# Optimization experiments

Measured on AMD Instinct MI355X. Metric: run time of the kernel, lower is better.

Reference implementation:

```python
import jax, jax.numpy as jnp
import numpy as np
from jax import lax

B, C, H, W = 8, 36, 256, 256
E, K, TD = 6, 2, 32
HID = C * 2  # ffn_expansion_factor = 2
EPS = 1e-10


def _conv3x3(x, w):
    # x: [B, Cin, H, W], w: [Cout, Cin, 3, 3], stride 1, pad 1, no bias
    return lax.conv_general_dilated(
        x, w, window_strides=(1, 1), padding=[(1, 1), (1, 1)],
        dimension_numbers=("NCHW", "OIHW", "NCHW"))


def _cv_squared(v):
    # torch .var() is unbiased (ddof=1)
    return jnp.var(v, ddof=1) / (jnp.mean(v) ** 2 + EPS)


def setup_inputs() -> dict:
    key = jax.random.key(0)
    ks = jax.random.split(key, 10)
    s = 0.05
    return {
        "x": jax.random.normal(ks[0], (B, C, H, W), dtype=jnp.float32),
        "time": jax.random.normal(ks[1], (B, TD), dtype=jnp.float32),
        # FeatureWiseAffine: Linear(time_dim -> expert_dim*2)
        "time_w": jax.random.normal(ks[2], (TD, HID), dtype=jnp.float32) * s,
        "time_b": jnp.zeros((HID,), dtype=jnp.float32),
        # gate: Linear(72,72) -> LeakyReLU -> Linear(72,6)
        "gate_w1": jax.random.normal(ks[3], (HID, HID), dtype=jnp.float32) * s,
        "gate_b1": jnp.zeros((HID,), dtype=jnp.float32),
        "gate_w2": jax.random.normal(ks[4], (HID, E), dtype=jnp.float32) * s,
        "gate_b2": jnp.zeros((E,), dtype=jnp.float32),
        # per-expert conv weights, stacked over experts
        "conv1_w": jax.random.normal(ks[5], (E, HID, C, 3, 3), dtype=jnp.float32) * s,
        "conv2_w": jax.random.normal(ks[6], (E, C, HID, 3, 3), dtype=jnp.float32) * s,
    }


def reference(x, time, time_w, time_b, gate_w1, gate_b1, gate_w2, gate_b2,
              conv1_w, conv2_w):
    # ---- gating (eval mode: no noise) ----
    # NOTE: source names are swapped: self.maxpool = AdaptiveAvgPool2d(1),
    # self.meanpool = AdaptiveMaxPool2d(1). Order preserved: [avg, max].
    avg_vec = jnp.mean(x, axis=(2, 3))              # [B, C]
    max_vec = jnp.max(x, axis=(2, 3))               # [B, C]
    v = jnp.concatenate([avg_vec, max_vec], axis=1)  # [B, 2C]
    v = v + time @ time_w + time_b                   # FeatureWiseAffine (additive)
    h = v @ gate_w1 + gate_b1
    h = jnp.where(h > 0, h, 0.01 * h)                # LeakyReLU(0.01)
    clean_logits = h @ gate_w2 + gate_b2             # [B, E]

    top_vals, top_idx = lax.top_k(clean_logits, min(K + 1, E))
    topk_gates = jax.nn.softmax(top_vals[:, :K], axis=1)     # [B, K]
    rows = jnp.arange(B)[:, None]
    gates = jnp.zeros_like(clean_logits).at[rows, top_idx[:, :K]].set(topk_gates)

    importance = gates.sum(axis=0)                           # [E]
    load = (gates > 0).sum(axis=0).astype(jnp.float32)       # [E] (eval path)
    loss = (_cv_squared(importance) + _cv_squared(load)) * 0.01

    # ---- dense equivalent of sparse dispatch / expert / gate-weighted combine ----
    # y[b] = sum_e gates[b,e] * expert_e(x[b]); zero gates contribute nothing,
    # identical to SparseDispatcher's gather -> conv -> scatter-add combine.
    y = jnp.zeros_like(x)
    for e in range(E):
        t = _conv3x3(x, conv1_w[e])
        t = jax.nn.gelu(t, approximate=False)   # F.gelu default = exact erf
        t = _conv3x3(t, conv2_w[e])
        y = y + gates[:, e].reshape(B, 1, 1, 1) * t
    return y, loss
```

## Files before the change

kernel.cpp:

```cpp
#include <hip/hip_runtime.h>
#include <hip/hip_bf16.h>
#include <math.h>

#define BB 8
#define CCH 36
#define HH 256
#define WW 256
#define EE 6
#define TDIM 32
#define HID 72
#define WS_GATES (BB*CCH*2)
#define WT1_OFF 4096
#define WT2_OFF (4096 + 368640)

#define TW 16
#define TH 8
#define XR 12
#define XC 20
#define TR 10
#define TC 18

typedef __attribute__((ext_vector_type(8))) short bf16x8;
typedef __attribute__((ext_vector_type(4))) float f32x4;

static __device__ __forceinline__ unsigned short f2bf(float f) {
  __hip_bfloat16 h = __float2bfloat16(f);
  return *(unsigned short*)&h;
}
static __device__ __forceinline__ float gelu_fast(float x) {
  float n2u = x * (-1.5957691216f - 0.0713548162f * x * x);
  float r = __builtin_amdgcn_rcpf(1.f + __expf(n2u));
  return x * r;
}

__global__ __launch_bounds__(256) void poolwx_kernel(const float* __restrict__ x,
                                                     const float* __restrict__ w1,
                                                     const float* __restrict__ w2,
                                                     float* __restrict__ ws,
                                                     unsigned short* __restrict__ wt1,
                                                     unsigned short* __restrict__ wt2) {
  if (blockIdx.x < 288) {
    const int bc = blockIdx.x;
    const float* p = x + (size_t)bc * (HH * WW);
    float s = 0.f, m = -INFINITY;
    for (int i = threadIdx.x; i < (HH * WW) / 4; i += 256) {
      float4 v = ((const float4*)p)[i];
      s += v.x + v.y + v.z + v.w;
      m = fmaxf(m, fmaxf(fmaxf(v.x, v.y), fmaxf(v.z, v.w)));
    }
    for (int off = 32; off; off >>= 1) {
      s += __shfl_down(s, off);
      m = fmaxf(m, __shfl_down(m, off));
    }
    __shared__ float ss[4], sm[4];
    int wid = threadIdx.x >> 6, lane = threadIdx.x & 63;
    if (lane == 0) { ss[wid] = s; sm[wid] = m; }
    __syncthreads();
    if (threadIdx.x == 0) {
      float S = ss[0] + ss[1] + ss[2] + ss[3];
      float M = fmaxf(fmaxf(sm[0], sm[1]), fmaxf(sm[2], sm[3]));
      ws[bc] = S * (1.f / (HH * WW));
      ws[BB * CCH + bc] = M;
    }
    return;
  }
  int i = (blockIdx.x - 288) * 256 + threadIdx.x;
  const int n1 = 360 * 512;
  if (i < n1) {
    int j = i & 7;
    int lane = (i >> 3) & 63;
    int f = i >> 9;
    int mt = f % 5;  f /= 5;
    int kc = f % 4;  f /= 4;
    int dx = f % 3;  int e = f / 3;
    int co = mt * 16 + (lane & 15);
    int k = kc * 32 + (lane >> 4) * 8 + j;
    int dy = k / 40, ci = k % 40;
    float v = 0.f;
    if (co < HID && k < 120 && ci < CCH)
      v = w1[(((size_t)(e * HID + co) * CCH + ci) * 3 + dy) * 3 + dx];
    wt1[i] = f2bf(v);
  }
  const int n2 = 378 * 512;
  if (i < n2) {
    int j = i & 7;
    int lane = (i >> 3) & 63;
    int f = i >> 9;
    int mt = f % 3;  f /= 3;
    int kc = f % 7;  f /= 7;
    int dx = f % 3;  int e = f / 3;
    int co = mt * 16 + (lane & 15);
    int k = kc * 32 + (lane >> 4) * 8 + j;
    int dy = k / 72, ci = k % 72;
    float v = 0.f;
    if (co < CCH && k < 216)
      v = w2[(((size_t)(e * CCH + co) * HID + ci) * 3 + dy) * 3 + dx];
    wt2[i] = f2bf(v);
  }
}

__global__ void gate_kernel(const float* __restrict__ time,
                            const float* __restrict__ time_w,
                            const float* __restrict__ time_b,
                            const float* __restrict__ w1, const float* __restrict__ b1,
                            const float* __restrict__ w2, const float* __restrict__ b2,
                            float* __restrict__ ws, float* __restrict__ loss_out) {
  __shared__ float v[BB * HID];
  __shared__ float h[BB * HID];
  __shared__ float logits[BB * EE];
  const int t = threadIdx.x;
  const float* avg = ws;
  const float* mx = ws + BB * CCH;
  for (int i = t; i < BB * HID; i += blockDim.x) {
    int b = i / HID, c = i % HID;
    float base = (c < CCH) ? avg[b * CCH + c] : mx[b * CCH + (c - CCH)];
    float acc = time_b[c];
    for (int k = 0; k < TDIM; k++) acc += time[b * TDIM + k] * time_w[k * HID + c];
    v[i] = base + acc;
  }
  __syncthreads();
  for (int i = t; i < BB * HID; i += blockDim.x) {
    int b = i / HID, c = i % HID;
    float acc = b1[c];
    for (int k = 0; k < HID; k++) acc += v[b * HID + k] * w1[k * HID + c];
    h[i] = acc > 0.f ? acc : 0.01f * acc;
  }
  __syncthreads();
  for (int i = t; i < BB * EE; i += blockDim.x) {
    int b = i / EE, e = i % EE;
    float acc = b2[e];
    for (int k = 0; k < HID; k++) acc += h[b * HID + k] * w2[k * EE + e];
    logits[i] = acc;
  }
  __syncthreads();
  if (t == 0) {
    float imp[EE], ld[EE];
    for (int e = 0; e < EE; e++) { imp[e] = 0.f; ld[e] = 0.f; }
    for (int b = 0; b < BB; b++) {
      int i1 = -1, i2 = -1;
      float v1 = -1e30f, v2 = -1e30f;
      for (int e = 0; e < EE; e++) {
        float lv = logits[b * EE + e];
        if (lv > v1) { v2 = v1; i2 = i1; v1 = lv; i1 = e; }
        else if (lv > v2) { v2 = lv; i2 = e; }
      }
      float e2 = expf(v2 - v1);
      float g1 = 1.f / (1.f + e2), g2 = e2 / (1.f + e2);
      for (int e = 0; e < EE; e++) ws[WS_GATES + b * EE + e] = 0.f;
      ws[WS_GATES + b * EE + i1] = g1;
      ws[WS_GATES + b * EE + i2] = g2;
      imp[i1] += g1; imp[i2] += g2;
      ld[i1] += 1.f; ld[i2] += 1.f;
    }
    float loss = 0.f;
    {
      float m = 0.f; for (int e = 0; e < EE; e++) m += imp[e]; m /= EE;
      float var = 0.f; for (int e = 0; e < EE; e++) { float d = imp[e] - m; var += d * d; }
      var /= (EE - 1);
      loss += var / (m * m + 1e-10f);
      m = 0.f; for (int e = 0; e < EE; e++) m += ld[e]; m /= EE;
      var = 0.f; for (int e = 0; e < EE; e++) { float d = ld[e] - m; var += d * d; }
      var /= (EE - 1);
      loss += var / (m * m + 1e-10f);
    }
    loss_out[0] = 0.01f * loss;
  }
}

__global__ __launch_bounds__(256, 3) void conv_kernel(
    const float* __restrict__ x,
    const unsigned short* __restrict__ wt1,
    const unsigned short* __restrict__ wt2,
    const float* __restrict__ wsg,
    float* __restrict__ y) {
  __shared__ __align__(16) char lds[48000];
  char* xsB = lds;
  char* tsB = lds + 19200;

  const int tid = threadIdx.x;
  const int w = tid >> 6;
  const int lane = tid & 63;
  const int l15 = lane & 15;
  const int kl = lane >> 4;
  const int b = blockIdx.y;
  const int tileId = (blockIdx.x & 7) * 64 + (blockIdx.x >> 3);
  const int tx0 = (tileId & 15) * TW;
  const int ty0 = (tileId >> 4) * TH;
  const size_t xbase = (size_t)b * (CCH * HH * WW);

  int eids[2] = {0, 0};
  float gvals[2] = {0.f, 0.f};
  int ne = 0;
  for (int e = 0; e < EE; e++) {
    float g = wsg[b * EE + e];
    if (g != 0.f && ne < 2) { eids[ne] = e; gvals[ne] = g; ne++; }
  }
  ne = __builtin_amdgcn_readfirstlane(ne);
  const int e0 = __builtin_amdgcn_readfirstlane(eids[0]);
  const int e1 = __builtin_amdgcn_readfirstlane(eids[1]);
  const float g0 = __int_as_float(__builtin_amdgcn_readfirstlane(__float_as_int(gvals[0])));
  const float g1 = __int_as_float(__builtin_amdgcn_readfirstlane(__float_as_int(gvals[1])));

  if (tid < XR * XC) {
    const int xr = tid / XC, xc = tid - (tid / XC) * XC;
    const int gy = ty0 - 2 + xr, gx = tx0 - 2 + xc;
    const bool valid = ((unsigned)gy < (unsigned)HH) && ((unsigned)gx < (unsigned)WW);
    const float* xp = x + xbase + (size_t)(gy * WW + gx);
    char* dstb = xsB + (xr * XC + xc) * 16;
#pragma unroll
    for (int c8 = 0; c8 < 5; c8++) {
      unsigned int pk[4];
#pragma unroll
      for (int q = 0; q < 4; q++) {
        int ci0 = c8 * 8 + q * 2, ci1 = ci0 + 1;
        float v0 = (ci0 < CCH && valid) ? xp[(size_t)ci0 << 16] : 0.f;
        float v1 = (ci1 < CCH && valid) ? xp[(size_t)ci1 << 16] : 0.f;
        pk[q] = (unsigned)f2bf(v0) | ((unsigned)f2bf(v1) << 16);
      }
      *(uint4*)(dstb + c8 * 3840) = make_uint4(pk[0], pk[1], pk[2], pk[3]);
    }
  }

  int vimg[3], pst[3], tsoff[3], pb1[3];
#pragma unroll
  for (int i = 0; i < 3; i++) {
    int p = (w + 4 * i) * 16 + l15;
    int tr = p / TC, tc = p - tr * TC;
    pst[i] = (p < TR * TC) ? 1 : 0;
    int trc = tr < (TR - 1) ? tr : (TR - 1);
    pb1[i] = trc * 320 + tc * 16;
    tsoff[i] = trc * 288 + tc * 16;
    int gy = ty0 - 1 + tr, gx = tx0 - 1 + tc;
    vimg[i] = (pst[i] && (unsigned)gy < (unsigned)HH && (unsigned)gx < (unsigned)WW) ? 1 : 0;
  }
  int b1a[4][3];
#pragma unroll
  for (int kc = 0; kc < 4; kc++) {
    int k0 = kc * 32 + kl * 8;
    int d = (k0 >= 80) ? 2 : (k0 >= 40 ? 1 : 0);
    int xkc = (k0 < 120) ? (((k0 - 40 * d) >> 3) * 3840 + d * 320) : 0;
#pragma unroll
    for (int i = 0; i < 3; i++) b1a[kc][i] = pb1[i] + xkc;
  }
  int tsStore[3];
#pragma unroll
  for (int i = 0; i < 3; i++) tsStore[i] = tsoff[i] + (kl >> 1) * 2880 + (kl & 1) * 8;

  int b2a[7][2];
#pragma unroll
  for (int kc = 0; kc < 7; kc++) {
    int k0 = kc * 32 + kl * 8;
    int d = (k0 >= 144) ? 2 : (k0 >= 72 ? 1 : 0);
    int tkc = (k0 < 216) ? (((k0 - 72 * d) >> 3) * 2880 + d * 288) : 0;
#pragma unroll
    for (int i = 0; i < 2; i++) b2a[kc][i] = (w + 4 * i) * 288 + l15 * 16 + tkc;
  }

  const int lob = lane * 8;

  f32x4 yacc[2][3];
#pragma unroll
  for (int i = 0; i < 2; i++)
#pragma unroll
    for (int mt = 0; mt < 3; mt++) yacc[i][mt] = (f32x4){0.f, 0.f, 0.f, 0.f};

  __syncthreads();

#pragma unroll
  for (int ei = 0; ei < 2; ei++) {
    if (ei >= ne) break;
    const float gv = ei ? g1 : g0;
    const unsigned short* w1p = wt1 + (ei ? e1 : e0) * 30720;
    const unsigned short* w2p = wt2 + (ei ? e1 : e0) * 32256;

    f32x4 acc[3][5];
#pragma unroll
    for (int i = 0; i < 3; i++)
#pragma unroll
      for (int mt = 0; mt < 5; mt++) acc[i][mt] = (f32x4){0.f, 0.f, 0.f, 0.f};

    bf16x8 aA[5], aB[5];
#pragma unroll
    for (int mt = 0; mt < 5; mt++) aA[mt] = *(const bf16x8*)(w1p + mt * 512 + lob);

#pragma unroll
    for (int jj = 0; jj < 12; jj++) {
      if (jj < 11) {
#pragma unroll
        for (int mt = 0; mt < 5; mt++)
          ((jj & 1) ? aA : aB)[mt] = *(const bf16x8*)(w1p + ((jj + 1) * 5 + mt) * 512 + lob);
      }
      const int kc = jj & 3;
      const int dxo = (jj >> 2) * 16;
      bf16x8 bv[3];
#pragma unroll
      for (int i = 0; i < 3; i++)
        bv[i] = *(const bf16x8*)(xsB + b1a[kc][i] + dxo);
      __builtin_amdgcn_s_setprio(1);
#pragma unroll
      for (int mt = 0; mt < 5; mt++) {
        bf16x8 av = ((jj & 1) ? aB : aA)[mt];
#pragma unroll
        for (int i = 0; i < 3; i++)
          acc[i][mt] = __builtin_amdgcn_mfma_f32_16x16x32_bf16(av, bv[i], acc[i][mt], 0, 0, 0);
      }
      __builtin_amdgcn_s_setprio(0);
    }

    bf16x8 c0[3], c1[3], c2[3];
#pragma unroll
    for (int mt = 0; mt < 3; mt++) {
      c0[mt] = *(const bf16x8*)(w2p + mt * 512 + lob);
      c1[mt] = *(const bf16x8*)(w2p + (3 + mt) * 512 + lob);
    }

#pragma unroll
    for (int i = 0; i < 3; i++) {
      if (pst[i]) {
#pragma unroll
        for (int mt = 0; mt < 5; mt++) {
          float v0 = vimg[i] ? gv * gelu_fast(acc[i][mt].x) : 0.f;
          float v1 = vimg[i] ? gv * gelu_fast(acc[i][mt].y) : 0.f;
          float v2 = vimg[i] ? gv * gelu_fast(acc[i][mt].z) : 0.f;
          float v3 = vimg[i] ? gv * gelu_fast(acc[i][mt].w) : 0.f;
          unsigned int lo = (unsigned)f2bf(v0) | ((unsigned)f2bf(v1) << 16);
          unsigned int hi = (unsigned)f2bf(v2) | ((unsigned)f2bf(v3) << 16);
          *(uint2*)(tsB + tsStore[i] + mt * 5760) = make_uint2(lo, hi);
        }
      }
    }
    __syncthreads();

#pragma unroll
    for (int jj = 0; jj < 21; jj++) {
      if (jj < 19) {
#pragma unroll
        for (int mt = 0; mt < 3; mt++) {
          bf16x8 v = *(const bf16x8*)(w2p + ((jj + 2) * 3 + mt) * 512 + lob);
          if ((jj % 3) == 0) c2[mt] = v;
          else if ((jj % 3) == 1) c0[mt] = v;
          else c1[mt] = v;
        }
      }
      const int kc = jj % 7;
      const int dxo = (jj / 7) * 16;
      bf16x8 bv[2];
#pragma unroll
      for (int i = 0; i < 2; i++)
        bv[i] = *(const bf16x8*)(tsB + b2a[kc][i] + dxo);
      __builtin_amdgcn_s_setprio(1);
#pragma unroll
      for (int mt = 0; mt < 3; mt++) {
        bf16x8 av = ((jj % 3) == 0) ? c0[mt] : ((jj % 3) == 1) ? c1[mt] : c2[mt];
#pragma unroll
        for (int i = 0; i < 2; i++)
          yacc[i][mt] = __builtin_amdgcn_mfma_f32_16x16x32_bf16(av, bv[i], yacc[i][mt], 0, 0, 0);
      }
      __builtin_amdgcn_s_setprio(0);
    }
    __syncthreads();
  }

#pragma unroll
  for (int i = 0; i < 2; i++) {
    int row = w + 4 * i;
#pragma unroll
    for (int mt = 0; mt < 3; mt++) {
#pragma unroll
      for (int r = 0; r < 4; r++) {
        int co = mt * 16 + kl * 4 + r;
        if (co < CCH) {
          float v = (r == 0) ? yacc[i][mt].x : (r == 1) ? yacc[i][mt].y
                  : (r == 2) ? yacc[i][mt].z : yacc[i][mt].w;
          y[xbase + ((size_t)co << 16) + (size_t)((ty0 + row) * WW + tx0 + l15)] = v;
        }
      }
    }
  }
}

extern "C" void kernel_launch(void* const* d_in, const int* in_sizes, int n_in,
                              void* d_out, int out_size, void* d_ws, size_t ws_size,
                              hipStream_t stream) {
  const float* x      = (const float*)d_in[0];
  const float* time   = (const float*)d_in[1];
  const float* time_w = (const float*)d_in[2];
  const float* time_b = (const float*)d_in[3];
  const float* gw1    = (const float*)d_in[4];
  const float* gb1    = (const float*)d_in[5];
  const float* gw2    = (const float*)d_in[6];
  const float* gb2    = (const float*)d_in[7];
  const float* w1     = (const float*)d_in[8];
  const float* w2     = (const float*)d_in[9];
  float* out = (float*)d_out;
  float* ws  = (float*)d_ws;
  unsigned short* wt1 = (unsigned short*)((char*)d_ws + WT1_OFF);
  unsigned short* wt2 = (unsigned short*)((char*)d_ws + WT2_OFF);

  hipLaunchKernelGGL(poolwx_kernel, dim3(288 + 756), dim3(256), 0, stream,
                     x, w1, w2, ws, wt1, wt2);
  hipLaunchKernelGGL(gate_kernel, dim3(1), dim3(128), 0, stream,
                     time, time_w, time_b, gw1, gb1, gw2, gb2,
                     ws, out + (size_t)(out_size - 1));
  hipLaunchKernelGGL(conv_kernel, dim3(512, BB), dim3(256), 0, stream,
                     x, wt1, wt2, ws + WS_GATES, out);
}
```

Baseline: 236.8 us.

## Stage expert conv weights in LDS via global_load_lds and alias x/t buffers

Weights for both convolutions are no longer read from global memory into registers by every wave. They are now staged in phases into a shared LDS weight buffer with direct global-to-LDS loads, and the MFMA loops read their A fragments from LDS. The x tile and the GELU intermediate tile now share one LDS region, so x is reloaded from global memory for each selected expert. This removes redundant per-wave global weight traffic and register double-buffering, at the cost of many extra __syncthreads between phases, loss of load/compute overlap, and a second global read of the x tile.

```diff
diff --git a/kernel.cpp b/kernel.cpp
--- a/kernel.cpp
+++ b/kernel.cpp
@@ -173,9 +173,10 @@
     const unsigned short* __restrict__ wt2,
     const float* __restrict__ wsg,
     float* __restrict__ y) {
-  __shared__ __align__(16) char lds[48000];
+  __shared__ __align__(16) char lds[49280];
   char* xsB = lds;
-  char* tsB = lds + 19200;
+  char* tsB = lds;
+  char* wB  = lds + 28800;
 
   const int tid = threadIdx.x;
   const int w = tid >> 6;
@@ -201,26 +202,6 @@
   const float g0 = __int_as_float(__builtin_amdgcn_readfirstlane(__float_as_int(gvals[0])));
   const float g1 = __int_as_float(__builtin_amdgcn_readfirstlane(__float_as_int(gvals[1])));
 
-  if (tid < XR * XC) {
-    const int xr = tid / XC, xc = tid - (tid / XC) * XC;
-    const int gy = ty0 - 2 + xr, gx = tx0 - 2 + xc;
-    const bool valid = ((unsigned)gy < (unsigned)HH) && ((unsigned)gx < (unsigned)WW);
-    const float* xp = x + xbase + (size_t)(gy * WW + gx);
-    char* dstb = xsB + (xr * XC + xc) * 16;
-#pragma unroll
-    for (int c8 = 0; c8 < 5; c8++) {
-      unsigned int pk[4];
-#pragma unroll
-      for (int q = 0; q < 4; q++) {
-        int ci0 = c8 * 8 + q * 2, ci1 = ci0 + 1;
-        float v0 = (ci0 < CCH && valid) ? xp[(size_t)ci0 << 16] : 0.f;
-        float v1 = (ci1 < CCH && valid) ? xp[(size_t)ci1 << 16] : 0.f;
-        pk[q] = (unsigned)f2bf(v0) | ((unsigned)f2bf(v1) << 16);
-      }
-      *(uint4*)(dstb + c8 * 3840) = make_uint4(pk[0], pk[1], pk[2], pk[3]);
-    }
-  }
-
   int vimg[3], pst[3], tsoff[3], pb1[3];
 #pragma unroll
   for (int i = 0; i < 3; i++) {
@@ -256,7 +237,7 @@
     for (int i = 0; i < 2; i++) b2a[kc][i] = (w + 4 * i) * 288 + l15 * 16 + tkc;
   }
 
-  const int lob = lane * 8;
+  const int lob = lane * 16;
 
   f32x4 yacc[2][3];
 #pragma unroll
@@ -264,14 +245,42 @@
 #pragma unroll
     for (int mt = 0; mt < 3; mt++) yacc[i][mt] = (f32x4){0.f, 0.f, 0.f, 0.f};
 
-  __syncthreads();
-
-#pragma unroll
   for (int ei = 0; ei < 2; ei++) {
     if (ei >= ne) break;
     const float gv = ei ? g1 : g0;
-    const unsigned short* w1p = wt1 + (ei ? e1 : e0) * 30720;
-    const unsigned short* w2p = wt2 + (ei ? e1 : e0) * 32256;
+    const char* w1p = (const char*)(wt1 + (ei ? e1 : e0) * 30720);
+    const char* w2p = (const char*)(wt2 + (ei ? e1 : e0) * 32256);
+
+    __syncthreads();
+
+#pragma unroll
+    for (int j = 0; j < 5; j++) {
+      int c = w + 4 * j;
+      __builtin_amdgcn_global_load_lds(
+          (const __attribute__((address_space(1))) void*)(w1p + c * 1024 + lob),
+          (__attribute__((address_space(3))) void*)(wB + c * 1024), 16, 0, 0);
+    }
+
+    if (tid < XR * XC) {
+      const int xr = tid / XC, xc = tid - (tid / XC) * XC;
+      const int gy = ty0 - 2 + xr, gx = tx0 - 2 + xc;
+      const bool valid = ((unsigned)gy < (unsigned)HH) && ((unsigned)gx < (unsigned)WW);
+      const float* xp = x + xbase + (size_t)(gy * WW + gx);
+      char* dstb = xsB + (xr * XC + xc) * 16;
+#pragma unroll
+      for (int c8 = 0; c8 < 5; c8++) {
+        unsigned int pk[4];
+#pragma unroll
+        for (int q = 0; q < 4; q++) {
+          int ci0 = c8 * 8 + q * 2, ci1 = ci0 + 1;
+          float v0 = (ci0 < CCH && valid) ? xp[(size_t)ci0 << 16] : 0.f;
+          float v1 = (ci1 < CCH && valid) ? xp[(size_t)ci1 << 16] : 0.f;
+          pk[q] = (unsigned)f2bf(v0) | ((unsigned)f2bf(v1) << 16);
+        }
+        *(uint4*)(dstb + c8 * 3840) = make_uint4(pk[0], pk[1], pk[2], pk[3]);
+      }
+    }
+    __syncthreads();
 
     f32x4 acc[3][5];
 #pragma unroll
@@ -279,39 +288,50 @@
 #pragma unroll
       for (int mt = 0; mt < 5; mt++) acc[i][mt] = (f32x4){0.f, 0.f, 0.f, 0.f};
 
-    bf16x8 aA[5], aB[5];
-#pragma unroll
-    for (int mt = 0; mt < 5; mt++) aA[mt] = *(const bf16x8*)(w1p + mt * 512 + lob);
-
-#pragma unroll
-    for (int jj = 0; jj < 12; jj++) {
-      if (jj < 11) {
+#pragma unroll
+    for (int ph = 0; ph < 3; ph++) {
+      if (ph > 0) {
+        __syncthreads();
+#pragma unroll
+        for (int j = 0; j < 5; j++) {
+          int c = w + 4 * j;
+          __builtin_amdgcn_global_load_lds(
+              (const __attribute__((address_space(1))) void*)(w1p + ph * 20480 + c * 1024 + lob),
+              (__attribute__((address_space(3))) void*)(wB + c * 1024), 16, 0, 0);
+        }
+        __syncthreads();
+      }
+#pragma unroll
+      for (int q = 0; q < 4; q++) {
+        const int jj = ph * 4 + q;
+        const int kc = jj & 3;
+        const int dxo = (jj >> 2) * 16;
+        bf16x8 bv[3];
+#pragma unroll
+        for (int i = 0; i < 3; i++)
+          bv[i] = *(const bf16x8*)(xsB + b1a[kc][i] + dxo);
+        bf16x8 av[5];
 #pragma unroll
         for (int mt = 0; mt < 5; mt++)
-          ((jj & 1) ? aA : aB)[mt] = *(const bf16x8*)(w1p + ((jj + 1) * 5 + mt) * 512 + lob);
-      }
-      const int kc = jj & 3;
-      const int dxo = (jj >> 2) * 16;
-      bf16x8 bv[3];
-#pragma unroll
-      for (int i = 0; i < 3; i++)
-        bv[i] = *(const bf16x8*)(xsB + b1a[kc][i] + dxo);
-      __builtin_amdgcn_s_setprio(1);
-#pragma unroll
-      for (int mt = 0; mt < 5; mt++) {
-        bf16x8 av = ((jj & 1) ? aB : aA)[mt];
-#pragma unroll
-        for (int i = 0; i < 3; i++)
-          acc[i][mt] = __builtin_amdgcn_mfma_f32_16x16x32_bf16(av, bv[i], acc[i][mt], 0, 0, 0);
-      }
-      __builtin_amdgcn_s_setprio(0);
-    }
-
-    bf16x8 c0[3], c1[3], c2[3];
-#pragma unroll
-    for (int mt = 0; mt < 3; mt++) {
-      c0[mt] = *(const bf16x8*)(w2p + mt * 512 + lob);
-      c1[mt] = *(const bf16x8*)(w2p + (3 + mt) * 512 + lob);
+          av[mt] = *(const bf16x8*)(wB + (q * 5 + mt) * 1024 + lob);
+        __builtin_amdgcn_s_setprio(1);
+#pragma unroll
+        for (int mt = 0; mt < 5; mt++)
+#pragma unroll
+          for (int i = 0; i < 3; i++)
+            acc[i][mt] = __builtin_amdgcn_mfma_f32_16x16x32_bf16(av[mt], bv[i], acc[i][mt], 0, 0, 0);
+        __builtin_amdgcn_s_setprio(0);
+      }
+    }
+
+    __syncthreads();
+#pragma unroll
+    for (int j = 0; j < 5; j++) {
+      int c = w + 4 * j;
+      if (c < 18)
+        __builtin_amdgcn_global_load_lds(
+            (const __attribute__((address_space(1))) void*)(w2p + c * 1024 + lob),
+            (__attribute__((address_space(3))) void*)(wB + c * 1024), 16, 0, 0);
     }
 
 #pragma unroll
@@ -332,33 +352,44 @@
     __syncthreads();
 
 #pragma unroll
-    for (int jj = 0; jj < 21; jj++) {
-      if (jj < 19) {
-#pragma unroll
-        for (int mt = 0; mt < 3; mt++) {
-          bf16x8 v = *(const bf16x8*)(w2p + ((jj + 2) * 3 + mt) * 512 + lob);
-          if ((jj % 3) == 0) c2[mt] = v;
-          else if ((jj % 3) == 1) c0[mt] = v;
-          else c1[mt] = v;
+    for (int ph = 0; ph < 4; ph++) {
+      if (ph > 0) {
+        __syncthreads();
+        const int cnt = (ph == 3) ? 9 : 18;
+#pragma unroll
+        for (int j = 0; j < 5; j++) {
+          int c = w + 4 * j;
+          if (c < cnt)
+            __builtin_amdgcn_global_load_lds(
+                (const __attribute__((address_space(1))) void*)(w2p + (ph * 18 + c) * 1024 + lob),
+                (__attribute__((address_space(3))) void*)(wB + c * 1024), 16, 0, 0);
         }
-      }
-      const int kc = jj % 7;
-      const int dxo = (jj / 7) * 16;
-      bf16x8 bv[2];
-#pragma unroll
-      for (int i = 0; i < 2; i++)
-        bv[i] = *(const bf16x8*)(tsB + b2a[kc][i] + dxo);
-      __builtin_amdgcn_s_setprio(1);
-#pragma unroll
-      for (int mt = 0; mt < 3; mt++) {
-        bf16x8 av = ((jj % 3) == 0) ? c0[mt] : ((jj % 3) == 1) ? c1[mt] : c2[mt];
+        __syncthreads();
+      }
+      const int nq = (ph == 3) ? 3 : 6;
+#pragma unroll
+      for (int q = 0; q < 6; q++) {
+        if (q >= nq) break;
+        const int jj = ph * 6 + q;
+        const int kc = jj % 7;
+        const int dxo = (jj / 7) * 16;
+        bf16x8 bv[2];
 #pragma unroll
         for (int i = 0; i < 2; i++)
-          yacc[i][mt] = __builtin_amdgcn_mfma_f32_16x16x32_bf16(av, bv[i], yacc[i][mt], 0, 0, 0);
-      }
-      __builtin_amdgcn_s_setprio(0);
-    }
-    __syncthreads();
+          bv[i] = *(const bf16x8*)(tsB + b2a[kc][i] + dxo);
+        bf16x8 av[3];
+#pragma unroll
+        for (int mt = 0; mt < 3; mt++)
+          av[mt] = *(const bf16x8*)(wB + (q * 3 + mt) * 1024 + lob);
+        __builtin_amdgcn_s_setprio(1);
+#pragma unroll
+        for (int mt = 0; mt < 3; mt++)
+#pragma unroll
+          for (int i = 0; i < 2; i++)
+            yacc[i][mt] = __builtin_amdgcn_mfma_f32_16x16x32_bf16(av[mt], bv[i], yacc[i][mt], 0, 0, 0);
+        __builtin_amdgcn_s_setprio(0);
+      }
+    }
   }
 
 #pragma unroll
```

Result: slower. 531.0 us (+124.2%).

## Stage expert weight fragments through double-buffered LDS shared by all waves

Applied to the files above, without the earlier changes.

Weight fragments used to be loaded per wave straight from global memory into registers. They are now loaded cooperatively by the four waves into a double-buffered LDS region and read back from LDS by every wave. The x tile and the GELU intermediate now share one LDS buffer, so the x tile is reloaded for each active expert. The aim is to cut redundant global and L2 weight traffic across waves. The cost is extra LDS reads, a __syncthreads in every pipeline stage, and a second x-tile load per block.

```diff
diff --git a/kernel.cpp b/kernel.cpp
--- a/kernel.cpp
+++ b/kernel.cpp
@@ -173,9 +173,10 @@
     const unsigned short* __restrict__ wt2,
     const float* __restrict__ wsg,
     float* __restrict__ y) {
-  __shared__ __align__(16) char lds[48000];
+  __shared__ __align__(16) char lds[49280];
   char* xsB = lds;
-  char* tsB = lds + 19200;
+  char* tsB = lds;
+  char* wB  = lds + 28800;
 
   const int tid = threadIdx.x;
   const int w = tid >> 6;
@@ -201,26 +202,6 @@
   const float g0 = __int_as_float(__builtin_amdgcn_readfirstlane(__float_as_int(gvals[0])));
   const float g1 = __int_as_float(__builtin_amdgcn_readfirstlane(__float_as_int(gvals[1])));
 
-  if (tid < XR * XC) {
-    const int xr = tid / XC, xc = tid - (tid / XC) * XC;
-    const int gy = ty0 - 2 + xr, gx = tx0 - 2 + xc;
-    const bool valid = ((unsigned)gy < (unsigned)HH) && ((unsigned)gx < (unsigned)WW);
-    const float* xp = x + xbase + (size_t)(gy * WW + gx);
-    char* dstb = xsB + (xr * XC + xc) * 16;
-#pragma unroll
-    for (int c8 = 0; c8 < 5; c8++) {
-      unsigned int pk[4];
-#pragma unroll
-      for (int q = 0; q < 4; q++) {
-        int ci0 = c8 * 8 + q * 2, ci1 = ci0 + 1;
-        float v0 = (ci0 < CCH && valid) ? xp[(size_t)ci0 << 16] : 0.f;
-        float v1 = (ci1 < CCH && valid) ? xp[(size_t)ci1 << 16] : 0.f;
-        pk[q] = (unsigned)f2bf(v0) | ((unsigned)f2bf(v1) << 16);
-      }
-      *(uint4*)(dstb + c8 * 3840) = make_uint4(pk[0], pk[1], pk[2], pk[3]);
-    }
-  }
-
   int vimg[3], pst[3], tsoff[3], pb1[3];
 #pragma unroll
   for (int i = 0; i < 3; i++) {
@@ -256,7 +237,7 @@
     for (int i = 0; i < 2; i++) b2a[kc][i] = (w + 4 * i) * 288 + l15 * 16 + tkc;
   }
 
-  const int lob = lane * 8;
+  const int lob16 = lane * 16;
 
   f32x4 yacc[2][3];
 #pragma unroll
@@ -264,14 +245,46 @@
 #pragma unroll
     for (int mt = 0; mt < 3; mt++) yacc[i][mt] = (f32x4){0.f, 0.f, 0.f, 0.f};
 
-  __syncthreads();
-
-#pragma unroll
+  bf16x8 r0, r1, r2;
+
   for (int ei = 0; ei < 2; ei++) {
     if (ei >= ne) break;
     const float gv = ei ? g1 : g0;
-    const unsigned short* w1p = wt1 + (ei ? e1 : e0) * 30720;
-    const unsigned short* w2p = wt2 + (ei ? e1 : e0) * 32256;
+    const char* w1p = (const char*)(wt1 + (ei ? e1 : e0) * 30720);
+    const char* w2p = (const char*)(wt2 + (ei ? e1 : e0) * 32256);
+
+    if (tid < XR * XC) {
+      const int xr = tid / XC, xc = tid - (tid / XC) * XC;
+      const int gy = ty0 - 2 + xr, gx = tx0 - 2 + xc;
+      const bool valid = ((unsigned)gy < (unsigned)HH) && ((unsigned)gx < (unsigned)WW);
+      const float* xp = x + xbase + (size_t)(gy * WW + gx);
+      char* dstb = xsB + (xr * XC + xc) * 16;
+#pragma unroll
+      for (int c8 = 0; c8 < 5; c8++) {
+        unsigned int pk[4];
+#pragma unroll
+        for (int q = 0; q < 4; q++) {
+          int ci0 = c8 * 8 + q * 2, ci1 = ci0 + 1;
+          float v0 = (ci0 < CCH && valid) ? xp[(size_t)ci0 << 16] : 0.f;
+          float v1 = (ci1 < CCH && valid) ? xp[(size_t)ci1 << 16] : 0.f;
+          pk[q] = (unsigned)f2bf(v0) | ((unsigned)f2bf(v1) << 16);
+        }
+        *(uint4*)(dstb + c8 * 3840) = make_uint4(pk[0], pk[1], pk[2], pk[3]);
+      }
+    }
+    {
+      int c0 = w, c1 = w + 4, c2 = w + 8;
+      r0 = *(const bf16x8*)(w1p + c0 * 1024 + lob16);
+      r1 = *(const bf16x8*)(w1p + c1 * 1024 + lob16);
+      if (c2 < 10) r2 = *(const bf16x8*)(w1p + c2 * 1024 + lob16);
+      *(bf16x8*)(wB + c0 * 1024 + lob16) = r0;
+      *(bf16x8*)(wB + c1 * 1024 + lob16) = r1;
+      if (c2 < 10) *(bf16x8*)(wB + c2 * 1024 + lob16) = r2;
+      r0 = *(const bf16x8*)(w1p + (10 + c0) * 1024 + lob16);
+      r1 = *(const bf16x8*)(w1p + (10 + c1) * 1024 + lob16);
+      if (c2 < 10) r2 = *(const bf16x8*)(w1p + (10 + c2) * 1024 + lob16);
+    }
+    __syncthreads();
 
     f32x4 acc[3][5];
 #pragma unroll
@@ -279,41 +292,62 @@
 #pragma unroll
       for (int mt = 0; mt < 5; mt++) acc[i][mt] = (f32x4){0.f, 0.f, 0.f, 0.f};
 
-    bf16x8 aA[5], aB[5];
-#pragma unroll
-    for (int mt = 0; mt < 5; mt++) aA[mt] = *(const bf16x8*)(w1p + mt * 512 + lob);
-
-#pragma unroll
-    for (int jj = 0; jj < 12; jj++) {
-      if (jj < 11) {
+#pragma unroll
+    for (int p = 0; p < 6; p++) {
+      {
+        char* dst = wB + ((p + 1) & 1) * 10240;
+        const int nfr = (p < 5) ? 10 : 9;
+        int c0 = w, c1 = w + 4, c2 = w + 8;
+        *(bf16x8*)(dst + c0 * 1024 + lob16) = r0;
+        *(bf16x8*)(dst + c1 * 1024 + lob16) = r1;
+        if (c2 < nfr) *(bf16x8*)(dst + c2 * 1024 + lob16) = r2;
+      }
+      {
+        int c0 = w, c1 = w + 4, c2 = w + 8;
+        if (p < 4) {
+          r0 = *(const bf16x8*)(w1p + ((p + 2) * 10 + c0) * 1024 + lob16);
+          r1 = *(const bf16x8*)(w1p + ((p + 2) * 10 + c1) * 1024 + lob16);
+          if (c2 < 10) r2 = *(const bf16x8*)(w1p + ((p + 2) * 10 + c2) * 1024 + lob16);
+        } else {
+          r0 = *(const bf16x8*)(w2p + ((p - 4) * 9 + c0) * 1024 + lob16);
+          r1 = *(const bf16x8*)(w2p + ((p - 4) * 9 + c1) * 1024 + lob16);
+          if (c2 < 9) r2 = *(const bf16x8*)(w2p + ((p - 4) * 9 + c2) * 1024 + lob16);
+        }
+      }
+      const char* wb = wB + (p & 1) * 10240;
+#pragma unroll
+      for (int s = 0; s < 2; s++) {
+        const int jj = 2 * p + s;
+        const int kc = jj & 3;
+        const int dxo = (jj >> 2) * 16;
+        bf16x8 bv[3];
+#pragma unroll
+        for (int i = 0; i < 3; i++)
+          bv[i] = *(const bf16x8*)(xsB + b1a[kc][i] + dxo);
+        bf16x8 av[5];
 #pragma unroll
         for (int mt = 0; mt < 5; mt++)
-          ((jj & 1) ? aA : aB)[mt] = *(const bf16x8*)(w1p + ((jj + 1) * 5 + mt) * 512 + lob);
-      }
-      const int kc = jj & 3;
-      const int dxo = (jj >> 2) * 16;
-      bf16x8 bv[3];
-#pragma unroll
-      for (int i = 0; i < 3; i++)
-        bv[i] = *(const bf16x8*)(xsB + b1a[kc][i] + dxo);
-      __builtin_amdgcn_s_setprio(1);
-#pragma unroll
-      for (int mt = 0; mt < 5; mt++) {
-        bf16x8 av = ((jj & 1) ? aB : aA)[mt];
-#pragma unroll
-        for (int i = 0; i < 3; i++)
-          acc[i][mt] = __builtin_amdgcn_mfma_f32_16x16x32_bf16(av, bv[i], acc[i][mt], 0, 0, 0);
-      }
-      __builtin_amdgcn_s_setprio(0);
-    }
-
-    bf16x8 c0[3], c1[3], c2[3];
-#pragma unroll
-    for (int mt = 0; mt < 3; mt++) {
-      c0[mt] = *(const bf16x8*)(w2p + mt * 512 + lob);
-      c1[mt] = *(const bf16x8*)(w2p + (3 + mt) * 512 + lob);
-    }
-
+          av[mt] = *(const bf16x8*)(wb + (s * 5 + mt) * 1024 + lob16);
+        __builtin_amdgcn_s_setprio(1);
+#pragma unroll
+        for (int mt = 0; mt < 5; mt++)
+#pragma unroll
+          for (int i = 0; i < 3; i++)
+            acc[i][mt] = __builtin_amdgcn_mfma_f32_16x16x32_bf16(av[mt], bv[i], acc[i][mt], 0, 0, 0);
+        __builtin_amdgcn_s_setprio(0);
+      }
+      __syncthreads();
+    }
+
+    {
+      int c0 = w, c1 = w + 4, c2 = w + 8;
+      *(bf16x8*)(wB + 10240 + c0 * 1024 + lob16) = r0;
+      *(bf16x8*)(wB + 10240 + c1 * 1024 + lob16) = r1;
+      if (c2 < 9) *(bf16x8*)(wB + 10240 + c2 * 1024 + lob16) = r2;
+      r0 = *(const bf16x8*)(w2p + (18 + c0) * 1024 + lob16);
+      r1 = *(const bf16x8*)(w2p + (18 + c1) * 1024 + lob16);
+      if (c2 < 9) r2 = *(const bf16x8*)(w2p + (18 + c2) * 1024 + lob16);
+    }
 #pragma unroll
     for (int i = 0; i < 3; i++) {
       if (pst[i]) {
@@ -332,33 +366,43 @@
     __syncthreads();
 
 #pragma unroll
-    for (int jj = 0; jj < 21; jj++) {
-      if (jj < 19) {
-#pragma unroll
-        for (int mt = 0; mt < 3; mt++) {
-          bf16x8 v = *(const bf16x8*)(w2p + ((jj + 2) * 3 + mt) * 512 + lob);
-          if ((jj % 3) == 0) c2[mt] = v;
-          else if ((jj % 3) == 1) c0[mt] = v;
-          else c1[mt] = v;
+    for (int q = 0; q < 7; q++) {
+      if (q >= 1 && q < 6) {
+        char* dst = wB + ((q + 1) & 1) * 10240;
+        int c0 = w, c1 = w + 4, c2 = w + 8;
+        *(bf16x8*)(dst + c0 * 1024 + lob16) = r0;
+        *(bf16x8*)(dst + c1 * 1024 + lob16) = r1;
+        if (c2 < 9) *(bf16x8*)(dst + c2 * 1024 + lob16) = r2;
+        if (q < 5) {
+          r0 = *(const bf16x8*)(w2p + ((q + 2) * 9 + c0) * 1024 + lob16);
+          r1 = *(const bf16x8*)(w2p + ((q + 2) * 9 + c1) * 1024 + lob16);
+          if (c2 < 9) r2 = *(const bf16x8*)(w2p + ((q + 2) * 9 + c2) * 1024 + lob16);
         }
       }
-      const int kc = jj % 7;
-      const int dxo = (jj / 7) * 16;
-      bf16x8 bv[2];
-#pragma unroll
-      for (int i = 0; i < 2; i++)
-        bv[i] = *(const bf16x8*)(tsB + b2a[kc][i] + dxo);
-      __builtin_amdgcn_s_setprio(1);
-#pragma unroll
-      for (int mt = 0; mt < 3; mt++) {
-        bf16x8 av = ((jj % 3) == 0) ? c0[mt] : ((jj % 3) == 1) ? c1[mt] : c2[mt];
+      const char* wb = wB + (q & 1) * 10240;
+#pragma unroll
+      for (int s = 0; s < 3; s++) {
+        const int jj = 3 * q + s;
+        const int kc = jj % 7;
+        const int dxo = (jj / 7) * 16;
+        bf16x8 bv[2];
 #pragma unroll
         for (int i = 0; i < 2; i++)
-          yacc[i][mt] = __builtin_amdgcn_mfma_f32_16x16x32_bf16(av, bv[i], yacc[i][mt], 0, 0, 0);
-      }
-      __builtin_amdgcn_s_setprio(0);
-    }
-    __syncthreads();
+          bv[i] = *(const bf16x8*)(tsB + b2a[kc][i] + dxo);
+        bf16x8 av[3];
+#pragma unroll
+        for (int mt = 0; mt < 3; mt++)
+          av[mt] = *(const bf16x8*)(wb + (s * 3 + mt) * 1024 + lob16);
+        __builtin_amdgcn_s_setprio(1);
+#pragma unroll
+        for (int mt = 0; mt < 3; mt++)
+#pragma unroll
+          for (int i = 0; i < 2; i++)
+            yacc[i][mt] = __builtin_amdgcn_mfma_f32_16x16x32_bf16(av[mt], bv[i], yacc[i][mt], 0, 0, 0);
+        __builtin_amdgcn_s_setprio(0);
+      }
+      __syncthreads();
+    }
   }
 
 #pragma unroll
```

After: 565.6 us. 139% more time.

## Split fused expert conv into two kernels with a bf16 intermediate in workspace

Applied to the files above, without the earlier changes.

Replaces the single fused conv1→GELU→conv2 kernel with two kernels whenever the workspace is large enough. The first runs conv1 only for the two selected experts per batch (16 slots), applies gate-scaled GELU and writes a bf16 channel-packed intermediate to global memory. The second reads both slots' intermediates with halos, accumulates conv2 for both experts in registers and writes the output. This avoids the halo recomputation and large LDS footprint of the fused tile, at the cost of roughly 150MB of extra global traffic for the intermediate.

```diff
diff --git a/kernel.cpp b/kernel.cpp
--- a/kernel.cpp
+++ b/kernel.cpp
@@ -10,8 +10,15 @@
 #define TDIM 32
 #define HID 72
 #define WS_GATES (BB*CCH*2)
+#define WS_EIDS  640
+#define WS_GVALS 656
 #define WT1_OFF 4096
 #define WT2_OFF (4096 + 368640)
+#define T_OFF   1048576
+#define SLOTSZ  (9*1048576)
+#define WS_NEEDED ((size_t)T_OFF + 16ull*SLOTSZ)
+
+#define ACH 4240
 
 #define TW 16
 #define TH 8
@@ -149,6 +156,8 @@
       for (int e = 0; e < EE; e++) ws[WS_GATES + b * EE + e] = 0.f;
       ws[WS_GATES + b * EE + i1] = g1;
       ws[WS_GATES + b * EE + i2] = g2;
+      ((int*)ws)[WS_EIDS + b * 2 + 0] = i1;  ws[WS_GVALS + b * 2 + 0] = g1;
+      ((int*)ws)[WS_EIDS + b * 2 + 1] = i2;  ws[WS_GVALS + b * 2 + 1] = g2;
       imp[i1] += g1; imp[i2] += g2;
       ld[i1] += 1.f; ld[i2] += 1.f;
     }
@@ -164,6 +173,228 @@
       loss += var / (m * m + 1e-10f);
     }
     loss_out[0] = 0.01f * loss;
+  }
+}
+
+__global__ __launch_bounds__(256, 4) void conv1_kernel(
+    const float* __restrict__ x,
+    const unsigned short* __restrict__ wt1,
+    const float* __restrict__ ws,
+    char* __restrict__ T) {
+  __shared__ __align__(16) char xs[5 * ACH];
+  const int tid = threadIdx.x;
+  const int w = tid >> 6;
+  const int lane = tid & 63;
+  const int l15 = lane & 15;
+  const int kl = lane >> 4;
+  const int y0 = (blockIdx.x >> 2) * 2;
+  const int x0 = (blockIdx.x & 3) * 64;
+  const int slot = blockIdx.y;
+  const int b = slot >> 1;
+  const size_t xbase = (size_t)b * (CCH * HH * WW);
+  const int eid = __builtin_amdgcn_readfirstlane(((const int*)ws)[WS_EIDS + slot]);
+  const float gv = __int_as_float(__builtin_amdgcn_readfirstlane(
+      __float_as_int(ws[WS_GVALS + slot])));
+
+#pragma unroll
+  for (int it = 0; it < 2; it++) {
+    int pos = tid + it * 256;
+    if (pos < 264) {
+      int r = pos / 66, c = pos - r * 66;
+      int gy = y0 - 1 + r, gx = x0 - 1 + c;
+      bool valid = ((unsigned)gy < (unsigned)HH) && ((unsigned)gx < (unsigned)WW);
+      const float* xp = x + xbase + (size_t)(gy * WW + gx);
+      char* dstb = xs + r * 1056 + c * 16;
+#pragma unroll
+      for (int c8 = 0; c8 < 5; c8++) {
+        unsigned int pk[4];
+#pragma unroll
+        for (int q = 0; q < 4; q++) {
+          int ci0 = c8 * 8 + q * 2, ci1 = ci0 + 1;
+          float v0 = (ci0 < CCH && valid) ? xp[(size_t)ci0 << 16] : 0.f;
+          float v1 = (ci1 < CCH && valid) ? xp[(size_t)ci1 << 16] : 0.f;
+          pk[q] = (unsigned)f2bf(v0) | ((unsigned)f2bf(v1) << 16);
+        }
+        *(uint4*)(dstb + c8 * ACH) = make_uint4(pk[0], pk[1], pk[2], pk[3]);
+      }
+    }
+  }
+
+  int b1a[4][2];
+#pragma unroll
+  for (int kc = 0; kc < 4; kc++) {
+    int k0 = kc * 32 + kl * 8;
+    int d = (k0 >= 80) ? 2 : (k0 >= 40 ? 1 : 0);
+    int xkc = (k0 < 120) ? ((k0 - 40 * d) >> 3) * ACH : 0;
+#pragma unroll
+    for (int i = 0; i < 2; i++)
+      b1a[kc][i] = xkc + (i + d) * 1056 + (w * 16 + l15) * 16;
+  }
+  const int lob = lane * 8;
+  const unsigned short* w1p = wt1 + eid * 30720;
+
+  f32x4 acc[2][5];
+#pragma unroll
+  for (int i = 0; i < 2; i++)
+#pragma unroll
+    for (int mt = 0; mt < 5; mt++) acc[i][mt] = (f32x4){0.f, 0.f, 0.f, 0.f};
+
+  __syncthreads();
+
+  bf16x8 aA[5], aB[5];
+#pragma unroll
+  for (int mt = 0; mt < 5; mt++) aA[mt] = *(const bf16x8*)(w1p + mt * 512 + lob);
+#pragma unroll
+  for (int jj = 0; jj < 12; jj++) {
+    if (jj < 11) {
+#pragma unroll
+      for (int mt = 0; mt < 5; mt++)
+        ((jj & 1) ? aA : aB)[mt] = *(const bf16x8*)(w1p + ((jj + 1) * 5 + mt) * 512 + lob);
+    }
+    const int kc = jj & 3;
+    const int dxo = (jj >> 2) * 16;
+    bf16x8 bv[2];
+#pragma unroll
+    for (int i = 0; i < 2; i++)
+      bv[i] = *(const bf16x8*)(xs + b1a[kc][i] + dxo);
+    __builtin_amdgcn_s_setprio(1);
+#pragma unroll
+    for (int mt = 0; mt < 5; mt++) {
+      bf16x8 av = ((jj & 1) ? aB : aA)[mt];
+#pragma unroll
+      for (int i = 0; i < 2; i++)
+        acc[i][mt] = __builtin_amdgcn_mfma_f32_16x16x32_bf16(av, bv[i], acc[i][mt], 0, 0, 0);
+    }
+    __builtin_amdgcn_s_setprio(0);
+  }
+
+  char* Ts = T + (size_t)slot * SLOTSZ;
+#pragma unroll
+  for (int i = 0; i < 2; i++) {
+    int p = (y0 + i) * 256 + x0 + w * 16 + l15;
+#pragma unroll
+    for (int mt = 0; mt < 5; mt++) {
+      if (mt < 4 || kl < 2) {
+        float v0 = gv * gelu_fast(acc[i][mt].x);
+        float v1 = gv * gelu_fast(acc[i][mt].y);
+        float v2 = gv * gelu_fast(acc[i][mt].z);
+        float v3 = gv * gelu_fast(acc[i][mt].w);
+        unsigned int lo = (unsigned)f2bf(v0) | ((unsigned)f2bf(v1) << 16);
+        unsigned int hi = (unsigned)f2bf(v2) | ((unsigned)f2bf(v3) << 16);
+        size_t addr = (size_t)(mt * 2 + (kl >> 1)) * 1048576 + (size_t)p * 16 + (kl & 1) * 8;
+        *(uint2*)(Ts + addr) = make_uint2(lo, hi);
+      }
+    }
+  }
+}
+
+__global__ __launch_bounds__(256, 4) void conv2_kernel(
+    const char* __restrict__ T,
+    const unsigned short* __restrict__ wt2,
+    const float* __restrict__ ws,
+    float* __restrict__ y) {
+  __shared__ __align__(16) char ts[9 * ACH];
+  const int tid = threadIdx.x;
+  const int w = tid >> 6;
+  const int lane = tid & 63;
+  const int l15 = lane & 15;
+  const int kl = lane >> 4;
+  const int y0 = (blockIdx.x >> 2) * 2;
+  const int x0 = (blockIdx.x & 3) * 64;
+  const int b = blockIdx.y;
+
+  int b2a[7][2];
+#pragma unroll
+  for (int kc = 0; kc < 7; kc++) {
+    int k0 = kc * 32 + kl * 8;
+    int d = (k0 >= 144) ? 2 : (k0 >= 72 ? 1 : 0);
+    int tkc = (k0 < 216) ? ((k0 - 72 * d) >> 3) * ACH : 0;
+#pragma unroll
+    for (int i = 0; i < 2; i++)
+      b2a[kc][i] = tkc + (i + d) * 1056 + (w * 16 + l15) * 16;
+  }
+  const int lob = lane * 8;
+
+  f32x4 yacc[2][3];
+#pragma unroll
+  for (int i = 0; i < 2; i++)
+#pragma unroll
+    for (int mt = 0; mt < 3; mt++) yacc[i][mt] = (f32x4){0.f, 0.f, 0.f, 0.f};
+
+  for (int ei = 0; ei < 2; ei++) {
+    const int slot = b * 2 + ei;
+    const int eid = __builtin_amdgcn_readfirstlane(((const int*)ws)[WS_EIDS + slot]);
+    const unsigned short* w2p = wt2 + eid * 32256;
+    const char* Ts = T + (size_t)slot * SLOTSZ;
+
+    if (ei) __syncthreads();
+#pragma unroll
+    for (int ch = 0; ch < 9; ch++) {
+#pragma unroll
+      for (int it = 0; it < 2; it++) {
+        int pos = tid + it * 256;
+        if (pos < 264) {
+          int r = pos / 66, c = pos - r * 66;
+          int gy = y0 - 1 + r, gx = x0 - 1 + c;
+          uint4 v = make_uint4(0, 0, 0, 0);
+          if ((unsigned)gy < (unsigned)HH && (unsigned)gx < (unsigned)WW)
+            v = *(const uint4*)(Ts + (size_t)ch * 1048576 + (size_t)(gy * 256 + gx) * 16);
+          *(uint4*)(ts + ch * ACH + r * 1056 + c * 16) = v;
+        }
+      }
+    }
+    __syncthreads();
+
+    bf16x8 c0[3], c1[3], c2[3];
+#pragma unroll
+    for (int mt = 0; mt < 3; mt++) {
+      c0[mt] = *(const bf16x8*)(w2p + mt * 512 + lob);
+      c1[mt] = *(const bf16x8*)(w2p + (3 + mt) * 512 + lob);
+    }
+#pragma unroll
+    for (int jj = 0; jj < 21; jj++) {
+      if (jj < 19) {
+#pragma unroll
+        for (int mt = 0; mt < 3; mt++) {
+          bf16x8 v = *(const bf16x8*)(w2p + ((jj + 2) * 3 + mt) * 512 + lob);
+          if ((jj % 3) == 0) c2[mt] = v;
+          else if ((jj % 3) == 1) c0[mt] = v;
+          else c1[mt] = v;
+        }
+      }
+      const int kc = jj % 7;
+      const int dxo = (jj / 7) * 16;
+      bf16x8 bv[2];
+#pragma unroll
+      for (int i = 0; i < 2; i++)
+        bv[i] = *(const bf16x8*)(ts + b2a[kc][i] + dxo);
+      __builtin_amdgcn_s_setprio(1);
+#pragma unroll
+      for (int mt = 0; mt < 3; mt++) {
+        bf16x8 av = ((jj % 3) == 0) ? c0[mt] : ((jj % 3) == 1) ? c1[mt] : c2[mt];
+#pragma unroll
+        for (int i = 0; i < 2; i++)
+          yacc[i][mt] = __builtin_amdgcn_mfma_f32_16x16x32_bf16(av, bv[i], yacc[i][mt], 0, 0, 0);
+      }
+      __builtin_amdgcn_s_setprio(0);
+    }
+  }
+
+  const size_t ybase = (size_t)b * (CCH * HH * WW);
+#pragma unroll
+  for (int i = 0; i < 2; i++) {
+#pragma unroll
+    for (int mt = 0; mt < 3; mt++) {
+#pragma unroll
+      for (int r = 0; r < 4; r++) {
+        int co = mt * 16 + kl * 4 + r;
+        if (co < CCH) {
+          float v = (r == 0) ? yacc[i][mt].x : (r == 1) ? yacc[i][mt].y
+                  : (r == 2) ? yacc[i][mt].z : yacc[i][mt].w;
+          y[ybase + ((size_t)co << 16) + (size_t)((y0 + i) * WW + x0 + w * 16 + l15)] = v;
+        }
+      }
+    }
   }
 }
 
@@ -402,6 +633,15 @@
   hipLaunchKernelGGL(gate_kernel, dim3(1), dim3(128), 0, stream,
                      time, time_w, time_b, gw1, gb1, gw2, gb2,
                      ws, out + (size_t)(out_size - 1));
-  hipLaunchKernelGGL(conv_kernel, dim3(512, BB), dim3(256), 0, stream,
-                     x, wt1, wt2, ws + WS_GATES, out);
-}
+
+  if (ws_size >= WS_NEEDED) {
+    char* T = (char*)d_ws + T_OFF;
+    hipLaunchKernelGGL(conv1_kernel, dim3(512, 16), dim3(256), 0, stream,
+                       x, wt1, ws, T);
+    hipLaunchKernelGGL(conv2_kernel, dim3(512, BB), dim3(256), 0, stream,
+                       T, wt2, ws, out);
+  } else {
+    hipLaunchKernelGGL(conv_kernel, dim3(512, BB), dim3(256), 0, stream,
+                       x, wt1, wt2, ws + WS_GATES, out);
+  }
+}
```

After: 375.2 us. 58.4% more time.
